# Kernel tuning notes

Measured on AMD Instinct MI355X. Metric: run time of the kernel, lower is better.

## Reference

```python
import jax, jax.numpy as jnp
import numpy as np

EMBED = 1024
HEADS = 16
HEAD_DIM = EMBED // HEADS
MLP_DIM = 4096
EPS = 1e-5


def setup_inputs() -> dict:
    key = jax.random.key(0)
    ks = jax.random.split(key, 12)
    s = lambda d: 1.0 / np.sqrt(d)
    return {
        "x": jax.random.normal(ks[0], (8, 1024, EMBED), dtype=jnp.float32),
        "ln1_g": jnp.ones((EMBED,), jnp.float32),
        "ln1_b": jnp.zeros((EMBED,), jnp.float32),
        "w_qkv": jax.random.normal(ks[1], (EMBED, 3 * EMBED), jnp.float32) * s(EMBED),
        "b_qkv": jnp.zeros((3 * EMBED,), jnp.float32),
        "w_proj": jax.random.normal(ks[2], (EMBED, EMBED), jnp.float32) * s(EMBED),
        "b_proj": jnp.zeros((EMBED,), jnp.float32),
        "ln2_g": jnp.ones((EMBED,), jnp.float32),
        "ln2_b": jnp.zeros((EMBED,), jnp.float32),
        "w_fc1": jax.random.normal(ks[3], (EMBED, MLP_DIM), jnp.float32) * s(EMBED),
        "b_fc1": jnp.zeros((MLP_DIM,), jnp.float32),
        "w_fc2": jax.random.normal(ks[4], (MLP_DIM, EMBED), jnp.float32) * s(MLP_DIM),
        "b_fc2": jnp.zeros((EMBED,), jnp.float32),
    }


def _layernorm(x, g, b):
    mu = jnp.mean(x, axis=-1, keepdims=True)
    var = jnp.mean(jnp.square(x - mu), axis=-1, keepdims=True)
    return (x - mu) * jax.lax.rsqrt(var + EPS) * g + b


def reference(x, ln1_g, ln1_b, w_qkv, b_qkv, w_proj, b_proj,
              ln2_g, ln2_b, w_fc1, b_fc1, w_fc2, b_fc2):
    B, N, D = x.shape
    scale = HEAD_DIM ** -0.5

    # --- attention branch ---
    h = _layernorm(x, ln1_g, ln1_b)
    qkv = h @ w_qkv + b_qkv                       # [B,N,3D]
    qkv = qkv.reshape(B, N, 3, HEADS, HEAD_DIM)
    q, k, v = jnp.moveaxis(qkv, 2, 0)             # each [B,N,H,hd]
    attn = jnp.einsum('bqhd,bkhd->bhqk', q, k) * scale
    attn = jax.nn.softmax(attn, axis=-1)
    out = jnp.einsum('bhqk,bkhd->bqhd', attn, v).reshape(B, N, D)
    x = x + (out @ w_proj + b_proj)

    # --- MLP branch ---
    h = _layernorm(x, ln2_g, ln2_b)
    h = jax.nn.gelu(h @ w_fc1 + b_fc1, approximate=False)
    x = x + (h @ w_fc2 + b_fc2)
    return x
```

## Files before the change

kernel.cpp:

```cpp
#include <hip/hip_runtime.h>
#include <cstdint>


typedef unsigned short u16;
typedef short short8 __attribute__((ext_vector_type(8)));
typedef float floatx4 __attribute__((ext_vector_type(4)));

#define GLB(p) ((const __attribute__((address_space(1))) void*)(p))
#define LDSP(p) ((__attribute__((address_space(3))) void*)(p))

__device__ __forceinline__ u16 f2bf(float f) {
    uint32_t u = __float_as_uint(f);
    u += 0x7fffu + ((u >> 16) & 1u);
    return (u16)(u >> 16);
}
__device__ __forceinline__ uint32_t pack2(float a, float b) {
    return (uint32_t)f2bf(a) | ((uint32_t)f2bf(b) << 16);
}
__device__ __forceinline__ float fast_gelu(float v) {
    float u = v * (0.7978845608f + 0.0356774081f * v * v);
    float e = __expf(2.0f * u);
    float th = 1.0f - 2.0f * __builtin_amdgcn_rcpf(e + 1.0f);
    return 0.5f * v * (1.0f + th);
}

__global__ __launch_bounds__(256) void transpose_cast_kernel(
    const float* __restrict__ W, u16* __restrict__ Wt, int K, int N)
{
    __shared__ float tile[32][33];
    int n0 = blockIdx.x * 32, k0 = blockIdx.y * 32;
    int tx = threadIdx.x, ty = threadIdx.y;
    #pragma unroll
    for (int i = 0; i < 4; ++i)
        tile[ty + i * 8][tx] = W[(size_t)(k0 + ty + i * 8) * N + n0 + tx];
    __syncthreads();
    #pragma unroll
    for (int i = 0; i < 4; ++i)
        Wt[(size_t)(n0 + ty + i * 8) * K + k0 + tx] = f2bf(tile[tx][ty + i * 8]);
}

__global__ __launch_bounds__(256) void ln_kernel(
    const float* __restrict__ x, const float* __restrict__ gw,
    const float* __restrict__ bw, u16* __restrict__ out)
{
    const int row = blockIdx.x, tid = threadIdx.x;
    float4 v = ((const float4*)(x + (size_t)row * 1024))[tid];
    float s  = v.x + v.y + v.z + v.w;
    float ss = v.x * v.x + v.y * v.y + v.z * v.z + v.w * v.w;
    #pragma unroll
    for (int off = 32; off > 0; off >>= 1) {
        s  += __shfl_down(s, off);
        ss += __shfl_down(ss, off);
    }
    __shared__ float red[8];
    if ((tid & 63) == 0) { red[tid >> 6] = s; red[4 + (tid >> 6)] = ss; }
    __syncthreads();
    float S  = red[0] + red[1] + red[2] + red[3];
    float SS = red[4] + red[5] + red[6] + red[7];
    float mu  = S * (1.0f / 1024.0f);
    float var = SS * (1.0f / 1024.0f) - mu * mu;
    float rs  = rsqrtf(var + 1e-5f);
    float4 g4 = ((const float4*)gw)[tid];
    float4 b4 = ((const float4*)bw)[tid];
    u16* o = out + (size_t)row * 1024 + tid * 4;
    o[0] = f2bf((v.x - mu) * rs * g4.x + b4.x);
    o[1] = f2bf((v.y - mu) * rs * g4.y + b4.y);
    o[2] = f2bf((v.z - mu) * rs * g4.z + b4.z);
    o[3] = f2bf((v.w - mu) * rs * g4.w + b4.w);
}

__global__ __launch_bounds__(256) void add2_kernel(
    const float* __restrict__ a, const float* __restrict__ b,
    float* __restrict__ o, int n4)
{
    int i = blockIdx.x * 256 + threadIdx.x;
    const int stride = gridDim.x * 256;
    for (; i < n4; i += stride) {
        float4 va = ((const float4*)a)[i], vb = ((const float4*)b)[i];
        ((float4*)o)[i] = make_float4(va.x + vb.x, va.y + vb.y, va.z + vb.z, va.w + vb.w);
    }
}

#define MODE_BF16      0
#define MODE_BF16_GELU 1
#define MODE_F32_RES   2
#define MODE_QKV       3
#define MODE_F32_SPLIT 4

#define G8_BUF1 32768
#define G8_LDS_BYTES 131072

#define SB()    __builtin_amdgcn_sched_barrier(0)
#define BARR()  do { __builtin_amdgcn_s_barrier(); SB(); } while (0)
#define GATE2() do { asm volatile("s_waitcnt vmcnt(2)" ::: "memory"); SB(); } while (0)
#define WL0()   do { asm volatile("s_waitcnt lgkmcnt(0)" ::: "memory"); SB(); } while (0)

#define RDA(DST, BUFOFF, MH) \
    _Pragma("unroll") \
    for (int mt = 0; mt < 4; ++mt) \
        _Pragma("unroll") \
        for (int ks = 0; ks < 2; ++ks) \
            DST[mt][ks] = *(const short8*)&lds[(BUFOFF) + \
                (size_t)(wr * 128 + (MH) * 64 + mt * 16 + lc) * 64 + \
                (((ks * 4 + lg) ^ (lc & 7)) * 8)];

#define RDB(DST, BUFOFF, NH) \
    _Pragma("unroll") \
    for (int nn = 0; nn < 2; ++nn) \
        _Pragma("unroll") \
        for (int ks = 0; ks < 2; ++ks) \
            DST[nn][ks] = *(const short8*)&lds[(BUFOFF) + 16384 + \
                (size_t)(wc * 64 + (NH) * 32 + nn * 16 + lc) * 64 + \
                (((ks * 4 + lg) ^ (lc & 7)) * 8)];

#define MMAQ(MH, NH, FA, FB) \
    __builtin_amdgcn_s_setprio(1); \
    _Pragma("unroll") \
    for (int ks = 0; ks < 2; ++ks) \
        _Pragma("unroll") \
        for (int mt = 0; mt < 4; ++mt) \
            _Pragma("unroll") \
            for (int nn = 0; nn < 2; ++nn) \
                acc[(MH) * 4 + mt][(NH) * 2 + nn] = \
                    __builtin_amdgcn_mfma_f32_16x16x32_bf16( \
                        FA[mt][ks], FB[nn][ks], acc[(MH) * 4 + mt][(NH) * 2 + nn], 0, 0, 0); \
    __builtin_amdgcn_s_setprio(0);

template<int MODE>
__global__ __launch_bounds__(512, 2) void gemm8_kernel(
    const u16* __restrict__ A, const u16* __restrict__ Bt,
    const float* __restrict__ bias, const float* __restrict__ res,
    void* __restrict__ outv, u16* __restrict__ vt,
    int M, int N, int lda, int ldb, int K)
{
    extern __shared__ u16 lds[];
    const int tid = threadIdx.x;
    const int wave = tid >> 6, lane = tid & 63;
    const int lg = lane >> 4, lc = lane & 15;
    const int nx = gridDim.x, nwg = nx * gridDim.y;
    const int orig = blockIdx.y * nx + blockIdx.x;
    const int q = nwg >> 3, r = nwg & 7, xc = orig & 7, oo = orig >> 3;
    const int sid = (xc < r ? xc * (q + 1) : r * (q + 1) + (xc - r) * q) + oo;
    const int m0 = (sid / nx) * 256, n0 = (sid % nx) * 256;
    const int wr = wave >> 2, wc = wave & 3;
    const int zed = (MODE == MODE_F32_SPLIT) ? blockIdx.z : 0;
    if (MODE == MODE_F32_SPLIT && zed) { A += K; Bt += K; }

    floatx4 acc[8][4];
    #pragma unroll
    for (int i = 0; i < 8; ++i)
        #pragma unroll
        for (int j = 0; j < 4; ++j) acc[i][j] = floatx4{0.f, 0.f, 0.f, 0.f};

    const int srow = lane >> 3;
    const int schunk = (lane & 7) ^ srow;

    const u16* Abase = A  + (size_t)(m0 + wave * 8 + srow) * lda + schunk * 8;
    const u16* Bbase = Bt + (size_t)(n0 + wave * 8 + srow) * ldb + schunk * 8;

    auto stageH = [&](int b, int o, int h, int kk) {
        if (o == 0) {
            const u16* src = Abase + (size_t)h * 128 * lda + kk;
            u16* dst = lds + b * G8_BUF1 + h * 8192 + wave * 512;
            __builtin_amdgcn_global_load_lds(GLB(src), LDSP(dst), 16, 0, 0);
            __builtin_amdgcn_global_load_lds(GLB(src + (size_t)64 * lda), LDSP(dst + 4096), 16, 0, 0);
        } else {
            const u16* src = Bbase + (size_t)h * 128 * ldb + kk;
            u16* dst = lds + b * G8_BUF1 + 16384 + h * 8192 + wave * 512;
            __builtin_amdgcn_global_load_lds(GLB(src), LDSP(dst), 16, 0, 0);
            __builtin_amdgcn_global_load_lds(GLB(src + (size_t)64 * ldb), LDSP(dst + 4096), 16, 0, 0);
        }
    };

    const int nt = K >> 6;

    stageH(0, 0, 0, 0); stageH(0, 0, 1, 0); stageH(0, 1, 0, 0); stageH(0, 1, 1, 0);
    stageH(1, 0, 0, 64);
    GATE2(); BARR();

    short8 fa0[4][2], fa1[4][2], fb0[2][2], fb1[2][2];

    for (int t0 = 0; t0 < nt; t0 += 2) {
        const int kk1 = (t0 + 1) * 64;
        const int kk2 = ((t0 + 2 < nt) ? t0 + 2 : nt - 1) * 64;
        const int kk3 = ((t0 + 3 < nt) ? t0 + 3 : nt - 1) * 64;
        stageH(1, 0, 1, kk1);
        RDA(fa0, 0, 0) RDB(fb0, 0, 0) SB();
        BARR(); WL0();
        MMAQ(0, 0, fa0, fb0)
        stageH(1, 1, 0, kk1);
        RDA(fa1, 0, 1) SB();
        BARR(); WL0();
        MMAQ(1, 0, fa1, fb0)
        stageH(1, 1, 1, kk1);
        RDB(fb1, 0, 1) SB();
        BARR(); WL0();
        MMAQ(1, 1, fa1, fb1)
        stageH(0, 0, 0, kk2); GATE2();
        BARR();
        MMAQ(0, 1, fa0, fb1)
        stageH(0, 0, 1, kk2); stageH(0, 1, 0, kk2);
        RDA(fa0, G8_BUF1, 0) RDB(fb0, G8_BUF1, 0) SB();
        BARR(); WL0();
        MMAQ(0, 0, fa0, fb0)
        stageH(0, 1, 1, kk2);
        RDA(fa1, G8_BUF1, 1) SB();
        BARR(); WL0();
        MMAQ(1, 0, fa1, fb0)
        RDB(fb1, G8_BUF1, 1) SB();
        BARR(); WL0();
        MMAQ(1, 1, fa1, fb1)
        stageH(1, 0, 0, kk3); GATE2();
        BARR();
        MMAQ(0, 1, fa0, fb1)
    }
    asm volatile("s_waitcnt vmcnt(0)" ::: "memory");

    if (MODE == MODE_QKV && n0 >= 2048) {
        #pragma unroll
        for (int mt = 0; mt < 8; ++mt) {
            #pragma unroll
            for (int nn = 0; nn < 4; ++nn) {
                const int col = n0 + wc * 64 + nn * 16 + lc;
                const float bv = bias[col];
                const int hd = col - 2048;
                const int rowbase = m0 + wr * 128 + mt * 16 + lg * 4;
                const int b = rowbase >> 10, token = rowbase & 1023;
                float v0 = acc[mt][nn][0] + bv, v1 = acc[mt][nn][1] + bv;
                float v2 = acc[mt][nn][2] + bv, v3 = acc[mt][nn][3] + bv;
                uint2 pk = {pack2(v0, v1), pack2(v2, v3)};
                *(uint2*)&vt[((size_t)b * 1024 + hd) * 1024 + token] = pk;
            }
        }
        return;
    }
    float* osel = (MODE == MODE_F32_SPLIT && zed) ? (float*)vt : (float*)outv;
    #pragma unroll
    for (int mt = 0; mt < 8; ++mt) {
        #pragma unroll
        for (int nn = 0; nn < 4; ++nn) {
            const int col = n0 + wc * 64 + nn * 16 + lc;
            const float bv = (MODE == MODE_F32_SPLIT && zed) ? 0.f : bias[col];
            #pragma unroll
            for (int r = 0; r < 4; ++r) {
                const int row = m0 + wr * 128 + mt * 16 + lg * 4 + r;
                float v = acc[mt][nn][r] + bv;
                if (MODE == MODE_BF16 || MODE == MODE_QKV) {
                    ((u16*)outv)[(size_t)row * N + col] = f2bf(v);
                } else if (MODE == MODE_BF16_GELU) {
                    ((u16*)outv)[(size_t)row * N + col] = f2bf(fast_gelu(v));
                } else if (MODE == MODE_F32_RES) {
                    ((float*)outv)[(size_t)row * N + col] = v + res[(size_t)row * N + col];
                } else {
                    osel[(size_t)row * N + col] = zed ? v : (v + res[(size_t)row * N + col]);
                }
            }
        }
    }
}

__global__ __launch_bounds__(256) void attn_kernel(
    const u16* __restrict__ qkv, const u16* __restrict__ vtg, u16* __restrict__ out)
{
    const int bid = blockIdx.x;
    const int g = ((bid >> 7) << 3) | (bid & 7);
    const int qt = (bid >> 3) & 15;
    const int h = g & 15, b = g >> 4;
    const int tid = threadIdx.x, wave = tid >> 6, lane = tid & 63;
    const int lg = lane >> 4, lc = lane & 15;

    __shared__ __attribute__((aligned(16))) u16 Qs[64 * 64];
    __shared__ __attribute__((aligned(16))) u16 Ks[64 * 64];
    __shared__ __attribute__((aligned(16))) u16 Vts[64 * 64];
    __shared__ __attribute__((aligned(16))) u16 Ps[64 * 64];

    const int q0 = qt * 64;
    const size_t hb = ((size_t)b * 1024) * 3072 + h * 64;
    const u16* vhead = vtg + ((size_t)b * 1024 + h * 64) * 1024;
    const int srow = lane >> 3;
    const int schunk = (lane & 7) ^ srow;

    {
        const u16* Qg = qkv + hb + (size_t)(q0 + wave * 16 + srow) * 3072 + schunk * 8;
        u16* Qw = &Qs[wave * 1024];
        __builtin_amdgcn_global_load_lds(GLB(Qg), LDSP(Qw), 16, 0, 0);
        __builtin_amdgcn_global_load_lds(GLB(Qg + (size_t)8 * 3072), LDSP(Qw + 512), 16, 0, 0);
    }
    __syncthreads();
    short8 aq[2];
    aq[0] = *(const short8*)&Qs[(wave * 16 + lc) * 64 + (((0 + lg) ^ (lc & 7)) * 8)];
    aq[1] = *(const short8*)&Qs[(wave * 16 + lc) * 64 + (((4 + lg) ^ (lc & 7)) * 8)];

    floatx4 o[4];
    #pragma unroll
    for (int dt = 0; dt < 4; ++dt) o[dt] = floatx4{0.f, 0.f, 0.f, 0.f};
    float mprev = -INFINITY, lsum = 0.f;
    const float sc = 0.125f;

    for (int kt = 0; kt < 16; ++kt) {
        __syncthreads();
        {
            const u16* Kg = qkv + hb + 1024 +
                (size_t)(kt * 64 + wave * 16 + srow) * 3072 + schunk * 8;
            u16* Kw = &Ks[wave * 1024];
            __builtin_amdgcn_global_load_lds(GLB(Kg), LDSP(Kw), 16, 0, 0);
            __builtin_amdgcn_global_load_lds(GLB(Kg + (size_t)8 * 3072), LDSP(Kw + 512), 16, 0, 0);
        }
        {
            const u16* Vg = vhead + (size_t)(wave * 16 + srow) * 1024 + kt * 64 + schunk * 8;
            u16* Vw = &Vts[wave * 1024];
            __builtin_amdgcn_global_load_lds(GLB(Vg), LDSP(Vw), 16, 0, 0);
            __builtin_amdgcn_global_load_lds(GLB(Vg + (size_t)8 * 1024), LDSP(Vw + 512), 16, 0, 0);
        }
        __syncthreads();

        floatx4 st[4];
        #pragma unroll
        for (int nt = 0; nt < 4; ++nt) st[nt] = floatx4{0.f, 0.f, 0.f, 0.f};
        #pragma unroll
        for (int ks = 0; ks < 2; ++ks)
            #pragma unroll
            for (int nt = 0; nt < 4; ++nt) {
                short8 fk = *(const short8*)&Ks[(nt * 16 + lc) * 64 +
                                                (((ks * 4 + lg) ^ (lc & 7)) * 8)];
                st[nt] = __builtin_amdgcn_mfma_f32_16x16x32_bf16(fk, aq[ks], st[nt], 0, 0, 0);
            }

        float m = st[0][0];
        #pragma unroll
        for (int nt = 0; nt < 4; ++nt)
            #pragma unroll
            for (int r = 0; r < 4; ++r) m = fmaxf(m, st[nt][r]);
        m = fmaxf(m, __shfl_xor(m, 16));
        m = fmaxf(m, __shfl_xor(m, 32));
        float mn = fmaxf(mprev, m * sc);
        float aexp = __expf(mprev - mn);
        mprev = mn;

        const int q = wave * 16 + lc;
        float rs = 0.f;
        #pragma unroll
        for (int nt = 0; nt < 4; ++nt) {
            float p0 = __expf(st[nt][0] * sc - mn);
            float p1 = __expf(st[nt][1] * sc - mn);
            float p2 = __expf(st[nt][2] * sc - mn);
            float p3 = __expf(st[nt][3] * sc - mn);
            rs += (p0 + p1) + (p2 + p3);
            const int c16 = nt * 2 + (lg >> 1);
            uint2 pk = {pack2(p0, p1), pack2(p2, p3)};
            *(uint2*)&Ps[q * 64 + ((c16 ^ (lc & 7)) * 8) + (lg & 1) * 4] = pk;
        }
        rs += __shfl_xor(rs, 16);
        rs += __shfl_xor(rs, 32);
        lsum = lsum * aexp + rs;
        #pragma unroll
        for (int dt = 0; dt < 4; ++dt)
            #pragma unroll
            for (int r = 0; r < 4; ++r) o[dt][r] *= aexp;

        #pragma unroll
        for (int ks = 0; ks < 2; ++ks) {
            short8 fp = *(const short8*)&Ps[q * 64 + (((ks * 4 + lg) ^ (lc & 7)) * 8)];
            #pragma unroll
            for (int dt = 0; dt < 4; ++dt) {
                short8 fv = *(const short8*)&Vts[(dt * 16 + lc) * 64 +
                                                 (((ks * 4 + lg) ^ (lc & 7)) * 8)];
                o[dt] = __builtin_amdgcn_mfma_f32_16x16x32_bf16(fv, fp, o[dt], 0, 0, 0);
            }
        }
    }

    const float rl = 1.0f / lsum;
    const int q = q0 + wave * 16 + lc;
    #pragma unroll
    for (int dt = 0; dt < 4; ++dt) {
        uint2 pk = {pack2(o[dt][0] * rl, o[dt][1] * rl),
                    pack2(o[dt][2] * rl, o[dt][3] * rl)};
        *(uint2*)&out[((size_t)b * 1024 + q) * 1024 + h * 64 + dt * 16 + lg * 4] = pk;
    }
}

extern "C" void kernel_launch(void* const* d_in, const int* in_sizes, int n_in,
                              void* d_out, int out_size, void* d_ws, size_t ws_size,
                              hipStream_t stream)
{
    const float* x      = (const float*)d_in[0];
    const float* ln1_g  = (const float*)d_in[1];
    const float* ln1_b  = (const float*)d_in[2];
    const float* w_qkv  = (const float*)d_in[3];
    const float* b_qkv  = (const float*)d_in[4];
    const float* w_proj = (const float*)d_in[5];
    const float* b_proj = (const float*)d_in[6];
    const float* ln2_g  = (const float*)d_in[7];
    const float* ln2_b  = (const float*)d_in[8];
    const float* w_fc1  = (const float*)d_in[9];
    const float* b_fc1  = (const float*)d_in[10];
    const float* w_fc2  = (const float*)d_in[11];
    const float* b_fc2  = (const float*)d_in[12];
    float* outp = (float*)d_out;

    char* ws = (char*)d_ws;
    size_t off = 0;
    auto alloc = [&](size_t bytes) { void* p = ws + off; off += (bytes + 255) & ~(size_t)255; return p; };
    u16*  wqkvT  = (u16*)alloc((size_t)3072 * 1024 * 2);
    u16*  wprojT = (u16*)alloc((size_t)1024 * 1024 * 2);
    u16*  wfc1T  = (u16*)alloc((size_t)4096 * 1024 * 2);
    u16*  hbuf   = (u16*)alloc((size_t)8192 * 1024 * 2);
    u16*  wfc2T  = (u16*)alloc((size_t)1024 * 4096 * 2);
    u16*  big    = (u16*)alloc((size_t)8192 * 4096 * 2);
    u16*  vtbuf  = (u16*)alloc((size_t)8 * 1024 * 1024 * 2);
    u16*  attno  = (u16*)alloc((size_t)8192 * 1024 * 2);
    float* x2    = (float*)alloc((size_t)8192 * 1024 * 4);
    float* p0    = (float*)vtbuf;
    float* p1    = (float*)wqkvT;

    static bool attr_done = []{
        hipFuncSetAttribute(reinterpret_cast<const void*>(gemm8_kernel<MODE_QKV>),
                            hipFuncAttributeMaxDynamicSharedMemorySize, G8_LDS_BYTES);
        hipFuncSetAttribute(reinterpret_cast<const void*>(gemm8_kernel<MODE_BF16_GELU>),
                            hipFuncAttributeMaxDynamicSharedMemorySize, G8_LDS_BYTES);
        hipFuncSetAttribute(reinterpret_cast<const void*>(gemm8_kernel<MODE_F32_RES>),
                            hipFuncAttributeMaxDynamicSharedMemorySize, G8_LDS_BYTES);
        hipFuncSetAttribute(reinterpret_cast<const void*>(gemm8_kernel<MODE_F32_SPLIT>),
                            hipFuncAttributeMaxDynamicSharedMemorySize, G8_LDS_BYTES);
        return true;
    }();
    (void)attr_done;

    dim3 tb(32, 8);
    transpose_cast_kernel<<<dim3(3072 / 32, 1024 / 32), tb, 0, stream>>>(w_qkv,  wqkvT,  1024, 3072);
    transpose_cast_kernel<<<dim3(1024 / 32, 1024 / 32), tb, 0, stream>>>(w_proj, wprojT, 1024, 1024);
    transpose_cast_kernel<<<dim3(4096 / 32, 1024 / 32), tb, 0, stream>>>(w_fc1,  wfc1T,  1024, 4096);
    transpose_cast_kernel<<<dim3(1024 / 32, 4096 / 32), tb, 0, stream>>>(w_fc2,  wfc2T,  4096, 1024);

    ln_kernel<<<8192, 256, 0, stream>>>(x, ln1_g, ln1_b, hbuf);
    gemm8_kernel<MODE_QKV><<<dim3(3072 / 256, 8192 / 256), 512, G8_LDS_BYTES, stream>>>(
        hbuf, wqkvT, b_qkv, nullptr, big, vtbuf, 8192, 3072, 1024, 1024, 1024);
    attn_kernel<<<2048, 256, 0, stream>>>(big, vtbuf, attno);
    gemm8_kernel<MODE_F32_RES><<<dim3(1024 / 256, 8192 / 256), 512, G8_LDS_BYTES, stream>>>(
        attno, wprojT, b_proj, x, x2, nullptr, 8192, 1024, 1024, 1024, 1024);
    ln_kernel<<<8192, 256, 0, stream>>>(x2, ln2_g, ln2_b, hbuf);
    gemm8_kernel<MODE_BF16_GELU><<<dim3(4096 / 256, 8192 / 256), 512, G8_LDS_BYTES, stream>>>(
        hbuf, wfc1T, b_fc1, nullptr, big, nullptr, 8192, 4096, 1024, 1024, 1024);
    gemm8_kernel<MODE_F32_SPLIT><<<dim3(1024 / 256, 8192 / 256, 2), 512, G8_LDS_BYTES, stream>>>(
        big, wfc2T, b_fc2, x2, p0, (u16*)p1, 8192, 1024, 4096, 4096, 2048);
    add2_kernel<<<2048, 256, 0, stream>>>(p0, p1, outp, 8192 * 1024 / 4);
}
```

Before: 500.5 us.

## Add 128x128 GEMM for N=1024 projections, drop split-K, double-buffer attention KV

Adds a smaller 128x128-tile, 4-wave GEMM kernel with double-buffered LDS staging. It is used for the proj and fc2 GEMMs (N=1024), giving 512 workgroups instead of 128, so fc2 no longer needs split-K plus a separate add kernel. The attention kernel now double-buffers K/V tiles with prefetch two tiles ahead and shares one LDS buffer between Q and P. Smaller tiles reuse less data per load, and the prefetch adds LDS usage and barriers.

```diff
diff --git a/kernel.cpp b/kernel.cpp
--- a/kernel.cpp
+++ b/kernel.cpp
@@ -69,23 +69,10 @@
     o[3] = f2bf((v.w - mu) * rs * g4.w + b4.w);
 }
 
-__global__ __launch_bounds__(256) void add2_kernel(
-    const float* __restrict__ a, const float* __restrict__ b,
-    float* __restrict__ o, int n4)
-{
-    int i = blockIdx.x * 256 + threadIdx.x;
-    const int stride = gridDim.x * 256;
-    for (; i < n4; i += stride) {
-        float4 va = ((const float4*)a)[i], vb = ((const float4*)b)[i];
-        ((float4*)o)[i] = make_float4(va.x + vb.x, va.y + vb.y, va.z + vb.z, va.w + vb.w);
-    }
-}
-
 #define MODE_BF16      0
 #define MODE_BF16_GELU 1
 #define MODE_F32_RES   2
 #define MODE_QKV       3
-#define MODE_F32_SPLIT 4
 
 #define G8_BUF1 32768
 #define G8_LDS_BYTES 131072
@@ -143,8 +130,6 @@
     const int sid = (xc < r ? xc * (q + 1) : r * (q + 1) + (xc - r) * q) + oo;
     const int m0 = (sid / nx) * 256, n0 = (sid % nx) * 256;
     const int wr = wave >> 2, wc = wave & 3;
-    const int zed = (MODE == MODE_F32_SPLIT) ? blockIdx.z : 0;
-    if (MODE == MODE_F32_SPLIT && zed) { A += K; Bt += K; }
 
     floatx4 acc[8][4];
     #pragma unroll
@@ -234,13 +219,12 @@
         }
         return;
     }
-    float* osel = (MODE == MODE_F32_SPLIT && zed) ? (float*)vt : (float*)outv;
     #pragma unroll
     for (int mt = 0; mt < 8; ++mt) {
         #pragma unroll
         for (int nn = 0; nn < 4; ++nn) {
             const int col = n0 + wc * 64 + nn * 16 + lc;
-            const float bv = (MODE == MODE_F32_SPLIT && zed) ? 0.f : bias[col];
+            const float bv = bias[col];
             #pragma unroll
             for (int r = 0; r < 4; ++r) {
                 const int row = m0 + wr * 128 + mt * 16 + lg * 4 + r;
@@ -249,10 +233,121 @@
                     ((u16*)outv)[(size_t)row * N + col] = f2bf(v);
                 } else if (MODE == MODE_BF16_GELU) {
                     ((u16*)outv)[(size_t)row * N + col] = f2bf(fast_gelu(v));
-                } else if (MODE == MODE_F32_RES) {
+                } else {
                     ((float*)outv)[(size_t)row * N + col] = v + res[(size_t)row * N + col];
+                }
+            }
+        }
+    }
+}
+
+#define G4_BUFSZ 16384
+#define G4_LDS_BYTES 65536
+
+template<int MODE>
+__global__ __launch_bounds__(256, 2) void gemm4_kernel(
+    const u16* __restrict__ A, const u16* __restrict__ Bt,
+    const float* __restrict__ bias, const float* __restrict__ res,
+    void* __restrict__ outv, u16* __restrict__ vt,
+    int M, int N, int lda, int ldb, int K)
+{
+    extern __shared__ u16 lds[];
+    const int tid = threadIdx.x;
+    const int wave = tid >> 6, lane = tid & 63;
+    const int lg = lane >> 4, lc = lane & 15;
+    const int nx = gridDim.x, nwg = nx * gridDim.y;
+    const int orig = blockIdx.y * nx + blockIdx.x;
+    const int q = nwg >> 3, r = nwg & 7, xc = orig & 7, oo = orig >> 3;
+    const int sid = (xc < r ? xc * (q + 1) : r * (q + 1) + (xc - r) * q) + oo;
+    const int m0 = (sid / nx) * 128, n0 = (sid % nx) * 128;
+    const int wr = wave >> 1, wc = wave & 1;
+
+    floatx4 acc[4][4];
+    #pragma unroll
+    for (int i = 0; i < 4; ++i)
+        #pragma unroll
+        for (int j = 0; j < 4; ++j) acc[i][j] = floatx4{0.f, 0.f, 0.f, 0.f};
+
+    const int srow = lane >> 3;
+    const int schunk = (lane & 7) ^ srow;
+
+    const u16* Agl = A  + (size_t)(m0 + wave * 32 + srow) * lda + schunk * 8;
+    const u16* Bgl = Bt + (size_t)(n0 + wave * 32 + srow) * ldb + schunk * 8;
+    const size_t a8 = (size_t)8 * lda, b8 = (size_t)8 * ldb;
+
+    const int nt = K >> 6;
+    auto stage = [&](int b, int kk) {
+        u16* base = lds + b * G4_BUFSZ;
+        #pragma unroll
+        for (int j = 0; j < 4; ++j)
+            __builtin_amdgcn_global_load_lds(GLB(Agl + kk + j * a8),
+                                             LDSP(base + (wave * 4 + j) * 512), 16, 0, 0);
+        #pragma unroll
+        for (int j = 0; j < 4; ++j)
+            __builtin_amdgcn_global_load_lds(GLB(Bgl + kk + j * b8),
+                                             LDSP(base + 8192 + (wave * 4 + j) * 512), 16, 0, 0);
+    };
+
+    stage(0, 0);
+    stage(1, 64);
+    asm volatile("s_waitcnt vmcnt(8)" ::: "memory");
+    __builtin_amdgcn_s_barrier();
+    __builtin_amdgcn_sched_barrier(0);
+
+    int cur = 0;
+    for (int t = 0; t < nt; ++t) {
+        const u16* Ab = lds + cur * G4_BUFSZ;
+        const u16* Bb = Ab + 8192;
+        #pragma unroll
+        for (int ks = 0; ks < 2; ++ks) {
+            short8 fa[4], fb[4];
+            #pragma unroll
+            for (int mt = 0; mt < 4; ++mt)
+                fa[mt] = *(const short8*)&Ab[(wr * 64 + mt * 16 + lc) * 64 +
+                                             (((ks * 4 + lg) ^ (lc & 7)) * 8)];
+            #pragma unroll
+            for (int nn = 0; nn < 4; ++nn)
+                fb[nn] = *(const short8*)&Bb[(wc * 64 + nn * 16 + lc) * 64 +
+                                             (((ks * 4 + lg) ^ (lc & 7)) * 8)];
+            __builtin_amdgcn_s_setprio(1);
+            #pragma unroll
+            for (int mt = 0; mt < 4; ++mt)
+                #pragma unroll
+                for (int nn = 0; nn < 4; ++nn)
+                    acc[mt][nn] = __builtin_amdgcn_mfma_f32_16x16x32_bf16(
+                        fa[mt], fb[nn], acc[mt][nn], 0, 0, 0);
+            __builtin_amdgcn_s_setprio(0);
+        }
+        asm volatile("s_waitcnt lgkmcnt(0)" ::: "memory");
+        __builtin_amdgcn_s_barrier();
+        __builtin_amdgcn_sched_barrier(0);
+        {
+            const int tn = (t + 2 < nt) ? t + 2 : nt - 1;
+            stage(cur, tn << 6);
+        }
+        asm volatile("s_waitcnt vmcnt(8)" ::: "memory");
+        __builtin_amdgcn_s_barrier();
+        __builtin_amdgcn_sched_barrier(0);
+        cur ^= 1;
+    }
+    asm volatile("s_waitcnt vmcnt(0)" ::: "memory");
+
+    #pragma unroll
+    for (int mt = 0; mt < 4; ++mt) {
+        #pragma unroll
+        for (int nn = 0; nn < 4; ++nn) {
+            const int col = n0 + wc * 64 + nn * 16 + lc;
+            const float bv = bias[col];
+            #pragma unroll
+            for (int r = 0; r < 4; ++r) {
+                const int row = m0 + wr * 64 + mt * 16 + lg * 4 + r;
+                float v = acc[mt][nn][r] + bv;
+                if (MODE == MODE_BF16) {
+                    ((u16*)outv)[(size_t)row * N + col] = f2bf(v);
+                } else if (MODE == MODE_BF16_GELU) {
+                    ((u16*)outv)[(size_t)row * N + col] = f2bf(fast_gelu(v));
                 } else {
-                    osel[(size_t)row * N + col] = zed ? v : (v + res[(size_t)row * N + col]);
+                    ((float*)outv)[(size_t)row * N + col] = v + res[(size_t)row * N + col];
                 }
             }
         }
@@ -269,10 +364,9 @@
     const int tid = threadIdx.x, wave = tid >> 6, lane = tid & 63;
     const int lg = lane >> 4, lc = lane & 15;
 
-    __shared__ __attribute__((aligned(16))) u16 Qs[64 * 64];
-    __shared__ __attribute__((aligned(16))) u16 Ks[64 * 64];
-    __shared__ __attribute__((aligned(16))) u16 Vts[64 * 64];
-    __shared__ __attribute__((aligned(16))) u16 Ps[64 * 64];
+    __shared__ __attribute__((aligned(16))) u16 Ks[2][64 * 64];
+    __shared__ __attribute__((aligned(16))) u16 Vts[2][64 * 64];
+    __shared__ __attribute__((aligned(16))) u16 QPs[64 * 64];
 
     const int q0 = qt * 64;
     const size_t hb = ((size_t)b * 1024) * 3072 + h * 64;
@@ -282,14 +376,30 @@
 
     {
         const u16* Qg = qkv + hb + (size_t)(q0 + wave * 16 + srow) * 3072 + schunk * 8;
-        u16* Qw = &Qs[wave * 1024];
+        u16* Qw = &QPs[wave * 1024];
         __builtin_amdgcn_global_load_lds(GLB(Qg), LDSP(Qw), 16, 0, 0);
         __builtin_amdgcn_global_load_lds(GLB(Qg + (size_t)8 * 3072), LDSP(Qw + 512), 16, 0, 0);
     }
-    __syncthreads();
+    auto stageKV = [&](int buf, int kt) {
+        const u16* Kg = qkv + hb + 1024 +
+            (size_t)(kt * 64 + wave * 16 + srow) * 3072 + schunk * 8;
+        u16* Kw = &Ks[buf][wave * 1024];
+        __builtin_amdgcn_global_load_lds(GLB(Kg), LDSP(Kw), 16, 0, 0);
+        __builtin_amdgcn_global_load_lds(GLB(Kg + (size_t)8 * 3072), LDSP(Kw + 512), 16, 0, 0);
+        const u16* Vg = vhead + (size_t)(wave * 16 + srow) * 1024 + kt * 64 + schunk * 8;
+        u16* Vw = &Vts[buf][wave * 1024];
+        __builtin_amdgcn_global_load_lds(GLB(Vg), LDSP(Vw), 16, 0, 0);
+        __builtin_amdgcn_global_load_lds(GLB(Vg + (size_t)8 * 1024), LDSP(Vw + 512), 16, 0, 0);
+    };
+    stageKV(0, 0);
+    stageKV(1, 1);
+    asm volatile("s_waitcnt vmcnt(4)" ::: "memory");
+    __builtin_amdgcn_s_barrier();
+    __builtin_amdgcn_sched_barrier(0);
+
     short8 aq[2];
-    aq[0] = *(const short8*)&Qs[(wave * 16 + lc) * 64 + (((0 + lg) ^ (lc & 7)) * 8)];
-    aq[1] = *(const short8*)&Qs[(wave * 16 + lc) * 64 + (((4 + lg) ^ (lc & 7)) * 8)];
+    aq[0] = *(const short8*)&QPs[(wave * 16 + lc) * 64 + (((0 + lg) ^ (lc & 7)) * 8)];
+    aq[1] = *(const short8*)&QPs[(wave * 16 + lc) * 64 + (((4 + lg) ^ (lc & 7)) * 8)];
 
     floatx4 o[4];
     #pragma unroll
@@ -297,23 +407,8 @@
     float mprev = -INFINITY, lsum = 0.f;
     const float sc = 0.125f;
 
+    int cur = 0;
     for (int kt = 0; kt < 16; ++kt) {
-        __syncthreads();
-        {
-            const u16* Kg = qkv + hb + 1024 +
-                (size_t)(kt * 64 + wave * 16 + srow) * 3072 + schunk * 8;
-            u16* Kw = &Ks[wave * 1024];
-            __builtin_amdgcn_global_load_lds(GLB(Kg), LDSP(Kw), 16, 0, 0);
-            __builtin_amdgcn_global_load_lds(GLB(Kg + (size_t)8 * 3072), LDSP(Kw + 512), 16, 0, 0);
-        }
-        {
-            const u16* Vg = vhead + (size_t)(wave * 16 + srow) * 1024 + kt * 64 + schunk * 8;
-            u16* Vw = &Vts[wave * 1024];
-            __builtin_amdgcn_global_load_lds(GLB(Vg), LDSP(Vw), 16, 0, 0);
-            __builtin_amdgcn_global_load_lds(GLB(Vg + (size_t)8 * 1024), LDSP(Vw + 512), 16, 0, 0);
-        }
-        __syncthreads();
-
         floatx4 st[4];
         #pragma unroll
         for (int nt = 0; nt < 4; ++nt) st[nt] = floatx4{0.f, 0.f, 0.f, 0.f};
@@ -321,8 +416,8 @@
         for (int ks = 0; ks < 2; ++ks)
             #pragma unroll
             for (int nt = 0; nt < 4; ++nt) {
-                short8 fk = *(const short8*)&Ks[(nt * 16 + lc) * 64 +
-                                                (((ks * 4 + lg) ^ (lc & 7)) * 8)];
+                short8 fk = *(const short8*)&Ks[cur][(nt * 16 + lc) * 64 +
+                                                    (((ks * 4 + lg) ^ (lc & 7)) * 8)];
                 st[nt] = __builtin_amdgcn_mfma_f32_16x16x32_bf16(fk, aq[ks], st[nt], 0, 0, 0);
             }
 
@@ -348,7 +443,7 @@
             rs += (p0 + p1) + (p2 + p3);
             const int c16 = nt * 2 + (lg >> 1);
             uint2 pk = {pack2(p0, p1), pack2(p2, p3)};
-            *(uint2*)&Ps[q * 64 + ((c16 ^ (lc & 7)) * 8) + (lg & 1) * 4] = pk;
+            *(uint2*)&QPs[q * 64 + ((c16 ^ (lc & 7)) * 8) + (lg & 1) * 4] = pk;
         }
         rs += __shfl_xor(rs, 16);
         rs += __shfl_xor(rs, 32);
@@ -360,15 +455,28 @@
 
         #pragma unroll
         for (int ks = 0; ks < 2; ++ks) {
-            short8 fp = *(const short8*)&Ps[q * 64 + (((ks * 4 + lg) ^ (lc & 7)) * 8)];
+            short8 fp = *(const short8*)&QPs[q * 64 + (((ks * 4 + lg) ^ (lc & 7)) * 8)];
             #pragma unroll
             for (int dt = 0; dt < 4; ++dt) {
-                short8 fv = *(const short8*)&Vts[(dt * 16 + lc) * 64 +
-                                                 (((ks * 4 + lg) ^ (lc & 7)) * 8)];
+                short8 fv = *(const short8*)&Vts[cur][(dt * 16 + lc) * 64 +
+                                                      (((ks * 4 + lg) ^ (lc & 7)) * 8)];
                 o[dt] = __builtin_amdgcn_mfma_f32_16x16x32_bf16(fv, fp, o[dt], 0, 0, 0);
             }
         }
-    }
+
+        asm volatile("s_waitcnt lgkmcnt(0)" ::: "memory");
+        __builtin_amdgcn_s_barrier();
+        __builtin_amdgcn_sched_barrier(0);
+        {
+            const int tn = (kt + 2 < 16) ? kt + 2 : 15;
+            stageKV(cur, tn);
+        }
+        asm volatile("s_waitcnt vmcnt(4)" ::: "memory");
+        __builtin_amdgcn_s_barrier();
+        __builtin_amdgcn_sched_barrier(0);
+        cur ^= 1;
+    }
+    asm volatile("s_waitcnt vmcnt(0)" ::: "memory");
 
     const float rl = 1.0f / lsum;
     const int q = q0 + wave * 16 + lc;
@@ -405,24 +513,20 @@
     u16*  wqkvT  = (u16*)alloc((size_t)3072 * 1024 * 2);
     u16*  wprojT = (u16*)alloc((size_t)1024 * 1024 * 2);
     u16*  wfc1T  = (u16*)alloc((size_t)4096 * 1024 * 2);
+    u16*  wfc2T  = (u16*)alloc((size_t)1024 * 4096 * 2);
     u16*  hbuf   = (u16*)alloc((size_t)8192 * 1024 * 2);
-    u16*  wfc2T  = (u16*)alloc((size_t)1024 * 4096 * 2);
     u16*  big    = (u16*)alloc((size_t)8192 * 4096 * 2);
     u16*  vtbuf  = (u16*)alloc((size_t)8 * 1024 * 1024 * 2);
     u16*  attno  = (u16*)alloc((size_t)8192 * 1024 * 2);
     float* x2    = (float*)alloc((size_t)8192 * 1024 * 4);
-    float* p0    = (float*)vtbuf;
-    float* p1    = (float*)wqkvT;
 
     static bool attr_done = []{
         hipFuncSetAttribute(reinterpret_cast<const void*>(gemm8_kernel<MODE_QKV>),
                             hipFuncAttributeMaxDynamicSharedMemorySize, G8_LDS_BYTES);
         hipFuncSetAttribute(reinterpret_cast<const void*>(gemm8_kernel<MODE_BF16_GELU>),
                             hipFuncAttributeMaxDynamicSharedMemorySize, G8_LDS_BYTES);
-        hipFuncSetAttribute(reinterpret_cast<const void*>(gemm8_kernel<MODE_F32_RES>),
-                            hipFuncAttributeMaxDynamicSharedMemorySize, G8_LDS_BYTES);
-        hipFuncSetAttribute(reinterpret_cast<const void*>(gemm8_kernel<MODE_F32_SPLIT>),
-                            hipFuncAttributeMaxDynamicSharedMemorySize, G8_LDS_BYTES);
+        hipFuncSetAttribute(reinterpret_cast<const void*>(gemm4_kernel<MODE_F32_RES>),
+                            hipFuncAttributeMaxDynamicSharedMemorySize, G4_LDS_BYTES);
         return true;
     }();
     (void)attr_done;
@@ -437,12 +541,11 @@
     gemm8_kernel<MODE_QKV><<<dim3(3072 / 256, 8192 / 256), 512, G8_LDS_BYTES, stream>>>(
         hbuf, wqkvT, b_qkv, nullptr, big, vtbuf, 8192, 3072, 1024, 1024, 1024);
     attn_kernel<<<2048, 256, 0, stream>>>(big, vtbuf, attno);
-    gemm8_kernel<MODE_F32_RES><<<dim3(1024 / 256, 8192 / 256), 512, G8_LDS_BYTES, stream>>>(
+    gemm4_kernel<MODE_F32_RES><<<dim3(1024 / 128, 8192 / 128), 256, G4_LDS_BYTES, stream>>>(
         attno, wprojT, b_proj, x, x2, nullptr, 8192, 1024, 1024, 1024, 1024);
     ln_kernel<<<8192, 256, 0, stream>>>(x2, ln2_g, ln2_b, hbuf);
     gemm8_kernel<MODE_BF16_GELU><<<dim3(4096 / 256, 8192 / 256), 512, G8_LDS_BYTES, stream>>>(
         hbuf, wfc1T, b_fc1, nullptr, big, nullptr, 8192, 4096, 1024, 1024, 1024);
-    gemm8_kernel<MODE_F32_SPLIT><<<dim3(1024 / 256, 8192 / 256, 2), 512, G8_LDS_BYTES, stream>>>(
-        big, wfc2T, b_fc2, x2, p0, (u16*)p1, 8192, 1024, 4096, 4096, 2048);
-    add2_kernel<<<2048, 256, 0, stream>>>(p0, p1, outp, 8192 * 1024 / 4);
-}
+    gemm4_kernel<MODE_F32_RES><<<dim3(1024 / 128, 8192 / 128), 256, G4_LDS_BYTES, stream>>>(
+        big, wfc2T, b_fc2, x2, outp, nullptr, 8192, 1024, 4096, 4096, 4096);
+}
```

New measurement: 474.9 us. 5.1% less time.
